# Optimization experiments

Measured on AMD Instinct MI355X. Metric: run time of the kernel, lower is better.

The kernel has to match this reference:

```python
import jax, jax.numpy as jnp
import numpy as np

SIZE = (160, 192, 160)  # matches init_kwargs `size`


def _make_grid(size):
    # torch: meshgrid(arange(s) for s, indexing='ij'), stack last dim, flip last dim
    vecs = [jnp.arange(s, dtype=jnp.float32) for s in size]
    g = jnp.stack(jnp.meshgrid(*vecs, indexing='ij'), axis=-1)
    g = g[..., ::-1]  # last-dim order becomes (x, y, z) = (W, H, D) indices
    return g[None]    # [1, D, H, W, 3]


def _grid_sample_3d(src, locs):
    """Trilinear grid_sample, align_corners=True, padding_mode='zeros'.
    src: [B, C, D, H, W]; locs: [B, D, H, W, 3] in [-1,1], last dim (x,y,z)."""
    B, C, D, H, W = src.shape
    dims_m1 = jnp.array([W - 1, H - 1, D - 1], jnp.float32)
    px = (locs + 1.0) * 0.5 * dims_m1  # unnormalize (align_corners=True)
    x, y, z = px[..., 0], px[..., 1], px[..., 2]
    x0 = jnp.floor(x); y0 = jnp.floor(y); z0 = jnp.floor(z)
    fx, fy, fz = x - x0, y - y0, z - z0
    x0i = x0.astype(jnp.int32); y0i = y0.astype(jnp.int32); z0i = z0.astype(jnp.int32)

    def gather(src_b, iz, iy, ix):  # src_b: [C,D,H,W]; idx: [D,H,W]
        return src_b[:, iz, iy, ix]  # [C,D,H,W]

    out = jnp.zeros(src.shape, src.dtype)
    for dz in (0, 1):
        for dy in (0, 1):
            for dx in (0, 1):
                ix, iy, iz = x0i + dx, y0i + dy, z0i + dz
                valid = (ix >= 0) & (ix < W) & (iy >= 0) & (iy < H) & (iz >= 0) & (iz < D)
                w = ((fx if dx else 1.0 - fx)
                     * (fy if dy else 1.0 - fy)
                     * (fz if dz else 1.0 - fz))
                w = jnp.where(valid, w, 0.0)  # zero padding for OOB
                icx = jnp.clip(ix, 0, W - 1)
                icy = jnp.clip(iy, 0, H - 1)
                icz = jnp.clip(iz, 0, D - 1)
                v = jax.vmap(gather)(src, icz, icy, icx)  # [B,C,D,H,W]
                out = out + w[:, None] * v
    return out


def setup_inputs() -> dict:
    key = jax.random.key(0)
    k1, k2 = jax.random.split(key)
    B, C = 2, 2
    D, H, W = SIZE
    src = jax.random.normal(k1, (B, C, D, H, W), dtype=jnp.float32)
    flow = jax.random.normal(k2, (B, 3, D, H, W), dtype=jnp.float32)
    return {"src": src, "flow": flow}


def reference(src, flow):
    # order='image': no flip of flow channels
    flow = jnp.moveaxis(flow, 1, -1)                      # [B,D,H,W,3]
    grid = _make_grid(SIZE)                                # [1,D,H,W,3]
    s = jnp.array(SIZE, jnp.float32)[::-1] - 1.0           # [W-1,H-1,D-1]
    new_locs = 2.0 * ((grid + flow) / s - 0.5)             # normalized [-1,1]
    return _grid_sample_3d(src, new_locs)
```

## Files before the change

### kernel.cpp

```cpp
#include <hip/hip_runtime.h>

#define DD 160
#define HH 192
#define WW 160
#define SP (DD * HH * WW)
#define NB 2
#define NC 2

#define TX 32
#define TY 8
#define TZ 8
#define RXW 40
#define RYH 15
#define RZD 15
#define REGC (RZD * RYH * RXW)
#define NCHUNK (REGC / 4)
#define NITER 5

#define NTX 5
#define NTY 24
#define NTZ 20
#define NTILES (NTX * NTY * NTZ * NB)
#define TPX (NTILES / 8)
#define NBLK 512

typedef float v2f __attribute__((ext_vector_type(2)));
typedef float v4f __attribute__((ext_vector_type(4)));

typedef const void __attribute__((address_space(1)))* gas_ptr;
typedef void __attribute__((address_space(3)))* las_ptr;

__device__ __forceinline__ v4f ld4_nt(const float* p) {
    return __builtin_nontemporal_load(reinterpret_cast<const v4f*>(p));
}
__device__ __forceinline__ void st4_nt(float* p, v4f v) {
    __builtin_nontemporal_store(v, reinterpret_cast<v4f*>(p));
}
__device__ __forceinline__ v2f ld2g(const float* p) {
    return *reinterpret_cast<const v2f*>(p);
}

__device__ __forceinline__ float sample_global1(
    const float* __restrict__ s,
    int x, int y, int z, float dx, float dy, float dz)
{
    float sx = (float)x + dx, sy = (float)y + dy, sz = (float)z + dz;
    float xf = floorf(sx), yf = floorf(sy), zf = floorf(sz);
    float fx = sx - xf, fy = sy - yf, fz = sz - zf;
    int x0 = (int)xf, y0 = (int)yf, z0 = (int)zf;
    int x1 = x0 + 1, y1 = y0 + 1, z1 = z0 + 1;

    float wx0 = (x0 >= 0 && x0 < WW) ? (1.0f - fx) : 0.0f;
    float wx1 = (x1 >= 0 && x1 < WW) ? fx : 0.0f;
    float wy0 = (y0 >= 0 && y0 < HH) ? (1.0f - fy) : 0.0f;
    float wy1 = (y1 >= 0 && y1 < HH) ? fy : 0.0f;
    float wz0 = (z0 >= 0 && z0 < DD) ? (1.0f - fz) : 0.0f;
    float wz1 = (z1 >= 0 && z1 < DD) ? fz : 0.0f;

    int p  = min(max(x0, 0), WW - 2);
    int i0 = min(max(x0, 0), WW - 1) - p;
    int i1 = min(max(x1, 0), WW - 1) - p;
    int cy0 = min(max(y0, 0), HH - 1), cy1 = min(max(y1, 0), HH - 1);
    int cz0 = min(max(z0, 0), DD - 1), cz1 = min(max(z1, 0), DD - 1);

    int o00 = (cz0 * HH + cy0) * WW + p;
    int o01 = (cz0 * HH + cy1) * WW + p;
    int o10 = (cz1 * HH + cy0) * WW + p;
    int o11 = (cz1 * HH + cy1) * WW + p;

    v2f c00 = ld2g(s + o00);
    v2f c01 = ld2g(s + o01);
    v2f c10 = ld2g(s + o10);
    v2f c11 = ld2g(s + o11);

    #define PICK(v, i) ((i) ? (v).y : (v).x)
    float r;
    r  = (wz0 * wy0) * (wx0 * PICK(c00, i0) + wx1 * PICK(c00, i1));
    r += (wz0 * wy1) * (wx0 * PICK(c01, i0) + wx1 * PICK(c01, i1));
    r += (wz1 * wy0) * (wx0 * PICK(c10, i0) + wx1 * PICK(c10, i1));
    r += (wz1 * wy1) * (wx0 * PICK(c11, i0) + wx1 * PICK(c11, i1));
    #undef PICK
    return r;
}

__device__ __forceinline__ void stage_channel(
    const float* __restrict__ cb, int X0, int Y0, int Z0, int tid, float* sbuf)
{
    #pragma unroll
    for (int i = 0; i < NITER; ++i) {
        int c = tid + i * 512;
        if (i < NITER - 1 || c < NCHUNK) {
            int lz  = c / 150;  int r2 = c - lz * 150;
            int ly  = r2 / 10;  int lxc = r2 - ly * 10;
            int mz = min(max(Z0 - 3 + lz, 0), DD - 1);
            int my = min(max(Y0 - 3 + ly, 0), HH - 1);
            int mx = min(max(X0 - 4 + lxc * 4, 0), WW - 4);
            const float* g = cb + (mz * HH + my) * WW + mx;
            __builtin_amdgcn_global_load_lds(
                (gas_ptr)g, (las_ptr)(sbuf + 4 * c), 16, 0, 0);
        }
    }
}

__device__ __forceinline__ float sample_lds(
    const float* __restrict__ sbuf,
    float lx, float ly, float lz, int rx0, int ry0, int rz0)
{
    float xf = floorf(lx), yf = floorf(ly), zf = floorf(lz);
    float fx = lx - xf, fy = ly - yf, fz = lz - zf;
    int ix = (int)xf, iy = (int)yf, iz = (int)zf;

    int vx0 = ix + rx0, vy0 = iy + ry0, vz0 = iz + rz0;
    float wx0 = (vx0 >= 0  && vx0 < WW)     ? (1.0f - fx) : 0.0f;
    float wx1 = (vx0 >= -1 && vx0 < WW - 1) ? fx          : 0.0f;
    float wy0 = (vy0 >= 0  && vy0 < HH)     ? (1.0f - fy) : 0.0f;
    float wy1 = (vy0 >= -1 && vy0 < HH - 1) ? fy          : 0.0f;
    float wz0 = (vz0 >= 0  && vz0 < DD)     ? (1.0f - fz) : 0.0f;
    float wz1 = (vz0 >= -1 && vz0 < DD - 1) ? fz          : 0.0f;

    const float* pB = sbuf + (iz * RYH + iy) * RXW + ix;
    float A00 = pB[0],        B00 = pB[1];
    float A01 = pB[RXW],      B01 = pB[RXW + 1];
    const float* pC = pB + RYH * RXW;
    float A10 = pC[0],        B10 = pC[1];
    float A11 = pC[RXW],      B11 = pC[RXW + 1];

    float c00 = wx0 * A00 + wx1 * B00;
    float c01 = wx0 * A01 + wx1 * B01;
    float c10 = wx0 * A10 + wx1 * B10;
    float c11 = wx0 * A11 + wx1 * B11;
    float m0  = wy0 * c00 + wy1 * c01;
    float m1  = wy0 * c10 + wy1 * c11;
    return wz0 * m0 + wz1 * m1;
}

struct Geo {
    int X0, Y0, Z0;
    int x, y, z;
    const float* sb;
    const float* fp;
    float* op;
};

__device__ __forceinline__ Geo decode_tile(
    int tl, const float* src, const float* flow, float* out,
    int xi, int yl, int zl)
{
    Geo g;
    int tx = tl % NTX;  int t2 = tl / NTX;
    int ty = t2 % NTY;  int t3 = t2 / NTY;
    int tz = t3 % NTZ;  int b  = t3 / NTZ;
    g.X0 = tx * TX; g.Y0 = ty * TY; g.Z0 = tz * TZ;
    g.x = g.X0 + xi; g.y = g.Y0 + yl; g.z = g.Z0 + zl;
    int go = (g.z * HH + g.y) * WW + g.x;
    g.sb = src + b * NC * SP;
    g.fp = flow + b * 3 * SP + go;
    g.op = out + b * NC * SP + go;
    return g;
}

__device__ __forceinline__ void compute_store(
    const float* __restrict__ sbuf, const Geo& g, int cofs,
    v4f dxv, v4f dyv, v4f dzv, int xi, int yl, int zl)
{
    const int rx0 = g.X0 - 4, ry0 = g.Y0 - 3, rz0 = g.Z0 - 3;
    float a[4];
    #pragma unroll
    for (int j = 0; j < 4; ++j) {
        float dx = dxv[j], dy = dyv[j], dz = dzv[j];
        bool inH = (dx >= -4.0f) & (dx < 4.0f) &
                   (dy >= -3.0f) & (dy < 4.0f) &
                   (dz >= -3.0f) & (dz < 4.0f);
        if (inH) {
            float lx = (float)(xi + j + 4) + dx;
            float ly = (float)(yl + 3) + dy;
            float lz = (float)(zl + 3) + dz;
            a[j] = sample_lds(sbuf, lx, ly, lz, rx0, ry0, rz0);
        } else {
            a[j] = sample_global1(g.sb + cofs, g.x + j, g.y, g.z, dx, dy, dz);
        }
    }
    v4f o = {a[0], a[1], a[2], a[3]};
    st4_nt(g.op + cofs, o);
}

__global__ __launch_bounds__(512, 4) void st_warp_kernel(
    const float* __restrict__ src,
    const float* __restrict__ flow,
    float* __restrict__ out)
{
    __shared__ float sA[REGC];
    __shared__ float sB[REGC];

    int u    = blockIdx.x;
    int xcd  = u & 7;
    int slot = u >> 3;
    int tid  = threadIdx.x;

    int rr = tid >> 3;
    int xi = (tid & 7) << 2;
    int yl = rr & 7, zl = rr >> 3;

    int nt = (TPX - slot + 63) >> 6;
    int tl = xcd * TPX + slot;

    Geo g = decode_tile(tl, src, flow, out, xi, yl, zl);
    stage_channel(g.sb, g.X0, g.Y0, g.Z0, tid, sA);
    v4f dxv = ld4_nt(g.fp);
    v4f dyv = ld4_nt(g.fp + SP);
    v4f dzv = ld4_nt(g.fp + 2 * SP);

    for (int t = 0; t < nt; ++t) {
        __syncthreads();

        stage_channel(g.sb + SP, g.X0, g.Y0, g.Z0, tid, sB);
        compute_store(sA, g, 0, dxv, dyv, dzv, xi, yl, zl);

        __syncthreads();

        bool more = (t + 1 < nt);
        Geo gn = g;
        v4f nxv = dxv, nyv = dyv, nzv = dzv;
        if (more) {
            gn = decode_tile(tl + ((t + 1) << 6), src, flow, out, xi, yl, zl);
            stage_channel(gn.sb, gn.X0, gn.Y0, gn.Z0, tid, sA);
            nxv = ld4_nt(gn.fp);
            nyv = ld4_nt(gn.fp + SP);
            nzv = ld4_nt(gn.fp + 2 * SP);
        }
        compute_store(sB, g, SP, dxv, dyv, dzv, xi, yl, zl);

        g = gn; dxv = nxv; dyv = nyv; dzv = nzv;
    }
}

extern "C" void kernel_launch(void* const* d_in, const int* in_sizes, int n_in,
                              void* d_out, int out_size, void* d_ws, size_t ws_size,
                              hipStream_t stream) {
    const float* src  = (const float*)d_in[0];
    const float* flow = (const float*)d_in[1];
    float* out = (float*)d_out;

    st_warp_kernel<<<NBLK, 512, 0, stream>>>(src, flow, out);
}
```

Measured before the change: 269.2 us.

## Halve tile depth, raise occupancy, add interior-tile fast path without bounds checks

Tile depth drops from 8 to 4 z-slices, so the LDS halo region shrinks (15 to 11 slices). That allows 6 blocks per CU and 768 blocks, with each thread handling 2 voxels instead of 4. A templated interior path skips the per-corner out-of-bounds weight masking for tiles whose halo is fully inside the volume. The trade-off is a worse halo-to-tile ratio, which means more redundant staged loads per output, and narrower vector loads and stores.

```diff
diff --git a/kernel.cpp b/kernel.cpp
--- a/kernel.cpp
+++ b/kernel.cpp
@@ -9,20 +9,21 @@
 
 #define TX 32
 #define TY 8
-#define TZ 8
+#define TZ 4
 #define RXW 40
 #define RYH 15
-#define RZD 15
+#define RZD 11
 #define REGC (RZD * RYH * RXW)
 #define NCHUNK (REGC / 4)
-#define NITER 5
+#define NITER 4
 
 #define NTX 5
 #define NTY 24
-#define NTZ 20
+#define NTZ 40
 #define NTILES (NTX * NTY * NTZ * NB)
 #define TPX (NTILES / 8)
-#define NBLK 512
+#define NBLK 768
+#define SLOTS (NBLK / 8)
 
 typedef float v2f __attribute__((ext_vector_type(2)));
 typedef float v4f __attribute__((ext_vector_type(4)));
@@ -30,11 +31,11 @@
 typedef const void __attribute__((address_space(1)))* gas_ptr;
 typedef void __attribute__((address_space(3)))* las_ptr;
 
-__device__ __forceinline__ v4f ld4_nt(const float* p) {
-    return __builtin_nontemporal_load(reinterpret_cast<const v4f*>(p));
-}
-__device__ __forceinline__ void st4_nt(float* p, v4f v) {
-    __builtin_nontemporal_store(v, reinterpret_cast<v4f*>(p));
+__device__ __forceinline__ v2f ld2_nt(const float* p) {
+    return __builtin_nontemporal_load(reinterpret_cast<const v2f*>(p));
+}
+__device__ __forceinline__ void st2_nt(float* p, v2f v) {
+    __builtin_nontemporal_store(v, reinterpret_cast<v2f*>(p));
 }
 __device__ __forceinline__ v2f ld2g(const float* p) {
     return *reinterpret_cast<const v2f*>(p);
@@ -102,6 +103,7 @@
     }
 }
 
+template<bool INTERIOR>
 __device__ __forceinline__ float sample_lds(
     const float* __restrict__ sbuf,
     float lx, float ly, float lz, int rx0, int ry0, int rz0)
@@ -110,13 +112,20 @@
     float fx = lx - xf, fy = ly - yf, fz = lz - zf;
     int ix = (int)xf, iy = (int)yf, iz = (int)zf;
 
-    int vx0 = ix + rx0, vy0 = iy + ry0, vz0 = iz + rz0;
-    float wx0 = (vx0 >= 0  && vx0 < WW)     ? (1.0f - fx) : 0.0f;
-    float wx1 = (vx0 >= -1 && vx0 < WW - 1) ? fx          : 0.0f;
-    float wy0 = (vy0 >= 0  && vy0 < HH)     ? (1.0f - fy) : 0.0f;
-    float wy1 = (vy0 >= -1 && vy0 < HH - 1) ? fy          : 0.0f;
-    float wz0 = (vz0 >= 0  && vz0 < DD)     ? (1.0f - fz) : 0.0f;
-    float wz1 = (vz0 >= -1 && vz0 < DD - 1) ? fz          : 0.0f;
+    float wx0, wx1, wy0, wy1, wz0, wz1;
+    if (INTERIOR) {
+        wx0 = 1.0f - fx; wx1 = fx;
+        wy0 = 1.0f - fy; wy1 = fy;
+        wz0 = 1.0f - fz; wz1 = fz;
+    } else {
+        int vx0 = ix + rx0, vy0 = iy + ry0, vz0 = iz + rz0;
+        wx0 = (vx0 >= 0  && vx0 < WW)     ? (1.0f - fx) : 0.0f;
+        wx1 = (vx0 >= -1 && vx0 < WW - 1) ? fx          : 0.0f;
+        wy0 = (vy0 >= 0  && vy0 < HH)     ? (1.0f - fy) : 0.0f;
+        wy1 = (vy0 >= -1 && vy0 < HH - 1) ? fy          : 0.0f;
+        wz0 = (vz0 >= 0  && vz0 < DD)     ? (1.0f - fz) : 0.0f;
+        wz1 = (vz0 >= -1 && vz0 < DD - 1) ? fz          : 0.0f;
+    }
 
     const float* pB = sbuf + (iz * RYH + iy) * RXW + ix;
     float A00 = pB[0],        B00 = pB[1];
@@ -137,6 +146,7 @@
 struct Geo {
     int X0, Y0, Z0;
     int x, y, z;
+    bool interior;
     const float* sb;
     const float* fp;
     float* op;
@@ -151,6 +161,9 @@
     int ty = t2 % NTY;  int t3 = t2 / NTY;
     int tz = t3 % NTZ;  int b  = t3 / NTZ;
     g.X0 = tx * TX; g.Y0 = ty * TY; g.Z0 = tz * TZ;
+    g.interior = (tx >= 1) & (tx <= 3) &
+                 (ty >= 1) & (ty <= 22) &
+                 (tz >= 1) & (tz <= 38);
     g.x = g.X0 + xi; g.y = g.Y0 + yl; g.z = g.Z0 + zl;
     int go = (g.z * HH + g.y) * WW + g.x;
     g.sb = src + b * NC * SP;
@@ -159,14 +172,15 @@
     return g;
 }
 
+template<bool INTERIOR>
 __device__ __forceinline__ void compute_store(
     const float* __restrict__ sbuf, const Geo& g, int cofs,
-    v4f dxv, v4f dyv, v4f dzv, int xi, int yl, int zl)
+    v2f dxv, v2f dyv, v2f dzv, int xi, int yl, int zl)
 {
     const int rx0 = g.X0 - 4, ry0 = g.Y0 - 3, rz0 = g.Z0 - 3;
-    float a[4];
+    float a[2];
     #pragma unroll
-    for (int j = 0; j < 4; ++j) {
+    for (int j = 0; j < 2; ++j) {
         float dx = dxv[j], dy = dyv[j], dz = dzv[j];
         bool inH = (dx >= -4.0f) & (dx < 4.0f) &
                    (dy >= -3.0f) & (dy < 4.0f) &
@@ -175,16 +189,16 @@
             float lx = (float)(xi + j + 4) + dx;
             float ly = (float)(yl + 3) + dy;
             float lz = (float)(zl + 3) + dz;
-            a[j] = sample_lds(sbuf, lx, ly, lz, rx0, ry0, rz0);
+            a[j] = sample_lds<INTERIOR>(sbuf, lx, ly, lz, rx0, ry0, rz0);
         } else {
             a[j] = sample_global1(g.sb + cofs, g.x + j, g.y, g.z, dx, dy, dz);
         }
     }
-    v4f o = {a[0], a[1], a[2], a[3]};
-    st4_nt(g.op + cofs, o);
-}
-
-__global__ __launch_bounds__(512, 4) void st_warp_kernel(
+    v2f o = {a[0], a[1]};
+    st2_nt(g.op + cofs, o);
+}
+
+__global__ __launch_bounds__(512, 6) void st_warp_kernel(
     const float* __restrict__ src,
     const float* __restrict__ flow,
     float* __restrict__ out)
@@ -197,38 +211,44 @@
     int slot = u >> 3;
     int tid  = threadIdx.x;
 
-    int rr = tid >> 3;
-    int xi = (tid & 7) << 2;
+    int xi = (tid & 15) << 1;
+    int rr = tid >> 4;
     int yl = rr & 7, zl = rr >> 3;
 
-    int nt = (TPX - slot + 63) >> 6;
+    int nt = (TPX - slot + SLOTS - 1) / SLOTS;
     int tl = xcd * TPX + slot;
 
     Geo g = decode_tile(tl, src, flow, out, xi, yl, zl);
     stage_channel(g.sb, g.X0, g.Y0, g.Z0, tid, sA);
-    v4f dxv = ld4_nt(g.fp);
-    v4f dyv = ld4_nt(g.fp + SP);
-    v4f dzv = ld4_nt(g.fp + 2 * SP);
+    v2f dxv = ld2_nt(g.fp);
+    v2f dyv = ld2_nt(g.fp + SP);
+    v2f dzv = ld2_nt(g.fp + 2 * SP);
 
     for (int t = 0; t < nt; ++t) {
         __syncthreads();
 
         stage_channel(g.sb + SP, g.X0, g.Y0, g.Z0, tid, sB);
-        compute_store(sA, g, 0, dxv, dyv, dzv, xi, yl, zl);
+        if (g.interior)
+            compute_store<true >(sA, g, 0, dxv, dyv, dzv, xi, yl, zl);
+        else
+            compute_store<false>(sA, g, 0, dxv, dyv, dzv, xi, yl, zl);
 
         __syncthreads();
 
         bool more = (t + 1 < nt);
         Geo gn = g;
-        v4f nxv = dxv, nyv = dyv, nzv = dzv;
+        v2f nxv = dxv, nyv = dyv, nzv = dzv;
         if (more) {
-            gn = decode_tile(tl + ((t + 1) << 6), src, flow, out, xi, yl, zl);
+            gn = decode_tile(tl + (t + 1) * SLOTS, src, flow, out, xi, yl, zl);
             stage_channel(gn.sb, gn.X0, gn.Y0, gn.Z0, tid, sA);
-            nxv = ld4_nt(gn.fp);
-            nyv = ld4_nt(gn.fp + SP);
-            nzv = ld4_nt(gn.fp + 2 * SP);
+            nxv = ld2_nt(gn.fp);
+            nyv = ld2_nt(gn.fp + SP);
+            nzv = ld2_nt(gn.fp + 2 * SP);
         }
-        compute_store(sB, g, SP, dxv, dyv, dzv, xi, yl, zl);
+        if (g.interior)
+            compute_store<true >(sB, g, SP, dxv, dyv, dzv, xi, yl, zl);
+        else
+            compute_store<false>(sB, g, SP, dxv, dyv, dzv, xi, yl, zl);
 
         g = gn; dxv = nxv; dyv = nyv; dzv = nzv;
     }
```

Result: slower. 280.8 us (+4.3%).
